# Performance work log

Hardware: AMD Instinct MI355X
Metric: run time of the kernel (lower is better)

The kernel has to match this reference:

```python
import jax, jax.numpy as jnp
from jax import lax
import numpy as np
import math

B, L = 256, 20000
HEADS, HEAD_DIM = 5, 30
W_POOL = (L - 10) // 5 + 1  # 3999, feature dim entering attention
ALPHA = 0.2  # tf.nn.leaky_relu default


def setup_inputs() -> dict:
    key = jax.random.key(0)
    ks = jax.random.split(key, 16)
    n = lambda k, shape: jax.random.normal(k, shape, dtype=jnp.float32) * 0.05
    return {
        "tokens": jax.random.randint(ks[0], (B, L), 0, 4, dtype=jnp.int32),
        "conv1_w": n(ks[1], (4, 10, 1, 5)),   # HWIO
        "conv1_b": jnp.zeros((5,), jnp.float32),
        "conv2_w": n(ks[2], (4, 10, 5, 1)),
        "conv2_b": jnp.zeros((1,), jnp.float32),
        "Wq": n(ks[3], (HEADS, W_POOL, HEAD_DIM)),
        "Wk": n(ks[4], (HEADS, W_POOL, HEAD_DIM)),
        "Wv": n(ks[5], (HEADS, W_POOL, HEAD_DIM)),
        "Wo": n(ks[6], (HEADS * HEAD_DIM, HEAD_DIM)),
        "d1_w": n(ks[7], (4 * HEAD_DIM, 10)),
        "d1_b": jnp.zeros((10,), jnp.float32),
        "d2_w": n(ks[8], (10, 10)),
        "d2_b": jnp.zeros((10,), jnp.float32),
        "d3_w": n(ks[9], (10, 1)),
        "d3_b": jnp.zeros((1,), jnp.float32),
    }


def _forward(tokens, conv1_w, conv1_b, conv2_w, conv2_b,
             Wq, Wk, Wv, Wo, d1_w, d1_b, d2_w, d2_b, d3_w, d3_b):
    dn = ("NHWC", "HWIO", "NHWC")
    # one_hot along axis 1: [B,4,L] -> NHWC image [B,4,L,1]
    x = jax.nn.one_hot(tokens, 4, axis=1, dtype=jnp.float32)[..., None]
    x = lax.conv_general_dilated(x, conv1_w, (1, 1), "SAME", dimension_numbers=dn) + conv1_b
    x = lax.conv_general_dilated(x, conv2_w, (1, 1), "SAME", dimension_numbers=dn) + conv2_b
    # MaxPool2D pool=(1,10), stride=(1,5), VALID -> [B,4,W_POOL,1]
    x = lax.reduce_window(x, -jnp.inf, lax.max, (1, 1, 10, 1), (1, 1, 5, 1), "VALID")
    x = x.reshape(x.shape[0], 4, -1)  # [B, S=4, D=W_POOL]
    S = x.shape[1]
    # batched multi-head causal self-attention (fused over heads)
    q = jnp.einsum("bsd,hde->bhse", x, Wq)
    k = jnp.einsum("bsd,hde->bhse", x, Wk)
    v = jnp.einsum("bsd,hde->bhse", x, Wv)
    scores = jnp.einsum("bhse,bhte->bhst", q, k) / math.sqrt(HEAD_DIM)
    mask = jnp.triu(jnp.full((S, S), -jnp.inf, dtype=jnp.float32), k=1)
    attn = jax.nn.softmax(scores + mask, axis=-1)
    o = jnp.einsum("bhst,bhte->bshe", attn, v).reshape(x.shape[0], S, HEADS * HEAD_DIM)
    o = o @ Wo  # [B, 4, 30]
    h = o.reshape(o.shape[0], -1)  # flatten -> [B, 120]
    h = jax.nn.leaky_relu(h @ d1_w + d1_b, ALPHA)
    h = jax.nn.leaky_relu(h @ d2_w + d2_b, ALPHA)
    return jax.nn.sigmoid(h @ d3_w + d3_b)  # [B, 1]


def reference(tokens, conv1_w, conv1_b, conv2_w, conv2_b,
              Wq, Wk, Wv, Wo, d1_w, d1_b, d2_w, d2_b, d3_w, d3_b):
    return _forward(tokens, conv1_w, conv1_b, conv2_w, conv2_b,
                    Wq, Wk, Wv, Wo, d1_w, d1_b, d2_w, d2_b, d3_w, d3_b)
```

## Files before the change

### kernel.cpp

```cpp
#include <hip/hip_runtime.h>
#include <math.h>

#define Bb 256
#define Ll 20000
#define WPOOL 3999
#define HEADS 5
#define HDIM 30
#define KSPLIT 8
#define NQKV 450
#define PSTRIDE (NQKV*1024)
#define BQT 4
#define WTRS 480
#define NB_K1 (Bb*16)

#define WS_F    0
#define WS_BIAS 368
#define WS_G    384
#define WS_FBL  1288
#define WS_FBR  2728
#define WS_BBL  4528
#define WS_BBR  4544
#define WS_X    4608
#define WS_P    (WS_X + Bb*WPOOL*4)
#define WS_WT   (WS_P + KSPLIT*PSTRIDE)

__device__ __forceinline__ float tbl_entry(const float* __restrict__ WP,
    int t, int d, int i, int kw2min, int kw2max)
{
    if (t >= 4) return 0.f;
    float p[4] = {0.f, 0.f, 0.f, 0.f};
#pragma unroll
    for (int kh = 0; kh < 4; ++kh) {
        int r = i + kh - 1;
        if (r < 0 || r > 3) continue;
        int kh1 = t - r + 1;
        if (kh1 < 0 || kh1 > 3) continue;
        int lo = d - kw2max; if (lo < 0) lo = 0;
        int hi = d - kw2min; if (hi > 9) hi = 9;
        const float* wpa = WP + (kh1 * 10) * 40 + kh * 10;
        for (int kw1 = lo; kw1 <= hi; ++kw1)
            p[kh] += wpa[kw1 * 40 + (d - kw1)];
    }
    return (p[0] + p[1]) + (p[2] + p[3]);
}

__global__ __launch_bounds__(256) void k0_build(const float* __restrict__ w1g,
    const float* __restrict__ b1g, const float* __restrict__ w2g,
    const float* __restrict__ b2g, float* __restrict__ ws)
{
    __shared__ float w1[200], w2[200], b1[5], WP[1600], SB[40], Fsh[360];
    __shared__ float b2v;
    const int tid = threadIdx.x;

    for (int i = tid; i < 200; i += 256) {
        w1[i] = w1g[i];
        w2[i] = w2g[i];
    }
    if (tid < 5) b1[tid] = b1g[tid];
    if (tid == 5) b2v = b2g[0];
    __syncthreads();

    for (int idx = tid; idx < 1600; idx += 256) {
        int a = idx / 40, b = idx % 40;
        float acc = 0.f;
#pragma unroll
        for (int c = 0; c < 5; ++c) acc += w1[a * 5 + c] * w2[b * 5 + c];
        WP[idx] = acc;
    }
    if (tid < 40) {
        float acc = 0.f;
#pragma unroll
        for (int c = 0; c < 5; ++c) acc += b1[c] * w2[tid * 5 + c];
        SB[tid] = acc;
    }
    __syncthreads();

    if (blockIdx.x == 0) {
        for (int idx = tid; idx < 360; idx += 256) {
            int t = idx / 72, d = (idx / 4) % 18, i = idx % 4;
            float v = tbl_entry(WP, t, d, i, 0, 9);
            Fsh[idx] = v;
            ws[WS_F + idx] = v;
        }
        if (tid < 4) {
            int i = tid;
            float acc = b2v;
#pragma unroll
            for (int kh = 0; kh < 4; ++kh) {
                int r = i + kh - 1;
                if (r < 0 || r > 3) continue;
                for (int kw2 = 0; kw2 < 10; ++kw2) acc += SB[kh * 10 + kw2];
            }
            ws[WS_BIAS + i] = acc;
        }
        __syncthreads();
        for (int idx = tid; idx < 900; idx += 256) {
            int p = idx / 36, j = (idx / 4) % 9, i = idx % 4;
            int t0 = p / 5, t1 = p % 5;
            ws[WS_G + idx] = Fsh[(t0 * 18 + 2 * j) * 4 + i]
                           + Fsh[(t1 * 18 + 2 * j + 1) * 4 + i];
        }
    } else {
        int gidx = (blockIdx.x - 1) * 256 + tid;
        if (gidx < 3240) {
            int wslot = gidx / 360, rem = gidx % 360;
            int t = rem / 72, d = (rem / 4) % 18, i = rem % 4;
            bool left = wslot < 4;
            int wloc = left ? wslot : wslot - 4;
            int kw2min = left ? 4 - wloc : 0;
            int kw2max = left ? 9 : 8 - wloc;
            float v = tbl_entry(WP, t, d, i, kw2min, kw2max);
            ws[(left ? WS_FBL + wloc * 360 : WS_FBR + wloc * 360) + rem] = v;
        } else if (gidx < 3276) {
            int bs = gidx - 3240;
            int wslot = bs / 4, i = bs % 4;
            bool left = wslot < 4;
            int wloc = left ? wslot : wslot - 4;
            int kw2min = left ? 4 - wloc : 0;
            int kw2max = left ? 9 : 8 - wloc;
            float acc = b2v;
#pragma unroll
            for (int kh = 0; kh < 4; ++kh) {
                int r = i + kh - 1;
                if (r < 0 || r > 3) continue;
                for (int kw2 = kw2min; kw2 <= kw2max; ++kw2)
                    acc += SB[kh * 10 + kw2];
            }
            ws[(left ? WS_BBL + wloc * 4 : WS_BBR + wloc * 4) + i] = acc;
        }
    }
}

__global__ __launch_bounds__(256) void k1_convpool(const int* __restrict__ tokens,
    const float* __restrict__ Wq, const float* __restrict__ Wk,
    const float* __restrict__ Wv, const float* __restrict__ ws_c,
    float* __restrict__ ws)
{
    __shared__ int tok[1280];
    __shared__ float4 Gs[225];
    __shared__ float4 m5[256];
    __shared__ float4 biasS;

    const int tid = threadIdx.x;

    if (blockIdx.x >= NB_K1) {
        int idx = (blockIdx.x - NB_K1) * 256 + tid;
        if (idx < WPOOL * WTRS) {
            int k = idx / WTRS, slot = idx % WTRS;
            int t = slot >> 2, c = slot & 3;
            int ph = t >> 3, j = t & 7;
            int proj = ph / 5, hh = ph % 5;
            float v = 0.f;
            int e = (j < 7) ? 4 * j + c : 28 + c;
            if (e < 30) {
                const float* Wm = (proj == 0) ? Wq : ((proj == 1) ? Wk : Wv);
                v = Wm[(size_t)hh * WPOOL * 30 + (size_t)k * 30 + e];
            }
            ws[WS_WT + idx] = v;
        }
        return;
    }

    const int b = blockIdx.x >> 4;
    const int chunk = blockIdx.x & 15;
    const int p0 = chunk * 250;
    const int pcnt = min(250, WPOOL - p0);
    const int colBase = 5 * p0 - 8;

    const float4* Gg = reinterpret_cast<const float4*>(ws_c + WS_G);
    for (int j = tid; j < 225; j += 256) Gs[j] = Gg[j];
    if (tid == 0) biasS = *reinterpret_cast<const float4*>(ws_c + WS_BIAS);
    const int* tb = tokens + (size_t)b * Ll;
    for (int j = tid; j < 1280; j += 256) {
        int u = colBase + j;
        tok[j] = (u >= 0 && u < Ll) ? tb[u] : 4;
    }
    __syncthreads();

    if (tid <= pcnt) {
        const int W = 5 * (p0 + tid);
        int tk[22];
#pragma unroll
        for (int m = 0; m < 22; ++m) tk[m] = tok[5 * tid + m];

        float4 mymax;
        const bool isLeft = (chunk == 0 && tid == 0);
        const bool isRight = (W + 4 >= Ll - 5);
        if (!isLeft && !isRight) {
            float4 bias4 = biasS;
            bool first = true;
#pragma unroll
            for (int c = 0; c < 5; ++c) {
                float a0 = bias4.x, a1 = bias4.y, a2 = bias4.z, a3 = bias4.w;
#pragma unroll
                for (int j = 0; j < 9; ++j) {
                    int pc = tk[c + 2 * j] * 5 + tk[c + 2 * j + 1];
                    float4 g = Gs[pc * 9 + j];
                    a0 += g.x; a1 += g.y; a2 += g.z; a3 += g.w;
                }
                if (first) { mymax = make_float4(a0, a1, a2, a3); first = false; }
                else {
                    mymax.x = fmaxf(mymax.x, a0); mymax.y = fmaxf(mymax.y, a1);
                    mymax.z = fmaxf(mymax.z, a2); mymax.w = fmaxf(mymax.w, a3);
                }
            }
        } else {
            bool first = true;
            for (int c = 0; c < 5; ++c) {
                int w = W + c;
                const float* T; const float* Bv;
                if (w < 4)            { T = ws_c + WS_FBL + w * 360;           Bv = ws_c + WS_BBL + 4 * w; }
                else if (w >= Ll - 5) { T = ws_c + WS_FBR + (w - (Ll - 5)) * 360; Bv = ws_c + WS_BBR + 4 * (w - (Ll - 5)); }
                else                  { T = ws_c + WS_F;                        Bv = ws_c + WS_BIAS; }
                float a0 = Bv[0], a1 = Bv[1], a2 = Bv[2], a3 = Bv[3];
                for (int d = 0; d < 18; ++d) {
                    const float* f = T + (size_t)(tk[c + d] * 18 + d) * 4;
                    a0 += f[0]; a1 += f[1]; a2 += f[2]; a3 += f[3];
                }
                if (first) { mymax = make_float4(a0, a1, a2, a3); first = false; }
                else {
                    mymax.x = fmaxf(mymax.x, a0); mymax.y = fmaxf(mymax.y, a1);
                    mymax.z = fmaxf(mymax.z, a2); mymax.w = fmaxf(mymax.w, a3);
                }
            }
        }
        m5[tid] = mymax;
    }
    __syncthreads();

    if (tid < pcnt) {
        float4 a = m5[tid], c = m5[tid + 1];
        a.x = fmaxf(a.x, c.x); a.y = fmaxf(a.y, c.y);
        a.z = fmaxf(a.z, c.z); a.w = fmaxf(a.w, c.w);
        reinterpret_cast<float4*>(ws + WS_X)[(size_t)b * WPOOL + p0 + tid] = a;
    }
}

__global__ __launch_bounds__(512) void k2_qkv(const float* __restrict__ xbuf,
    const float* __restrict__ wtbuf, float* __restrict__ ws)
{
    __shared__ float red[120 * 65];
    const int tid = threadIdx.x;
    const int ks = blockIdx.x & 7;
    const int bt = blockIdx.x >> 3;
    const int bq0 = bt * BQT;
    const int k0 = ks * 500;
    const int kn = min(500, WPOOL - k0);

    const int grp = tid >> 7;
    const int t = tid & 127;
    const int gk0 = __builtin_amdgcn_readfirstlane(grp) * 125;
    const int gend = min(gk0 + 125, kn);

    const int ph = t >> 3, j = t & 7;
    const int proj = ph / 5, hh = ph % 5;
    const int e0 = (j < 7) ? 4 * j : 28;
    const bool quad = (j < 7);
    const float* wt = wtbuf + (size_t)k0 * WTRS + 4 * t;
    const float4* xg[BQT];
#pragma unroll
    for (int b = 0; b < BQT; ++b)
        xg[b] = reinterpret_cast<const float4*>(xbuf)
                + (size_t)(bq0 + b) * WPOOL + k0;

    float acc[BQT][4][4] = {};

#define FMA_STEP(KIDX, W) do {                                       \
        _Pragma("unroll")                                            \
        for (int b = 0; b < BQT; ++b) {                              \
            float4 xv = xg[b][KIDX];                                 \
            acc[b][0][0] = fmaf(xv.x, W.x, acc[b][0][0]);            \
            acc[b][1][0] = fmaf(xv.y, W.x, acc[b][1][0]);            \
            acc[b][2][0] = fmaf(xv.z, W.x, acc[b][2][0]);            \
            acc[b][3][0] = fmaf(xv.w, W.x, acc[b][3][0]);            \
            acc[b][0][1] = fmaf(xv.x, W.y, acc[b][0][1]);            \
            acc[b][1][1] = fmaf(xv.y, W.y, acc[b][1][1]);            \
            acc[b][2][1] = fmaf(xv.z, W.y, acc[b][2][1]);            \
            acc[b][3][1] = fmaf(xv.w, W.y, acc[b][3][1]);            \
            acc[b][0][2] = fmaf(xv.x, W.z, acc[b][0][2]);            \
            acc[b][1][2] = fmaf(xv.y, W.z, acc[b][1][2]);            \
            acc[b][2][2] = fmaf(xv.z, W.z, acc[b][2][2]);            \
            acc[b][3][2] = fmaf(xv.w, W.z, acc[b][3][2]);            \
            acc[b][0][3] = fmaf(xv.x, W.w, acc[b][0][3]);            \
            acc[b][1][3] = fmaf(xv.y, W.w, acc[b][1][3]);            \
            acc[b][2][3] = fmaf(xv.z, W.w, acc[b][2][3]);            \
            acc[b][3][3] = fmaf(xv.w, W.w, acc[b][3][3]);            \
        }                                                            \
    } while (0)

    if (t < 120) {
        float4 wv[4];
#pragma unroll
        for (int i = 0; i < 4; ++i)
            wv[i] = *reinterpret_cast<const float4*>(wt + (size_t)(gk0 + i) * WTRS);

        int kk = gk0;
        for (; kk + 4 <= gend; kk += 4) {
#pragma unroll
            for (int i = 0; i < 4; ++i) {
                float4 W = wv[i];
                int nidx = kk + 4 + i;
                int ncl = nidx < gend ? nidx : gend - 1;
                wv[i] = *reinterpret_cast<const float4*>(wt + (size_t)ncl * WTRS);
                FMA_STEP(kk + i, W);
            }
        }
        for (; kk < gend; ++kk) {
            float4 W = *reinterpret_cast<const float4*>(wt + (size_t)kk * WTRS);
            FMA_STEP(kk, W);
        }
    }
#undef FMA_STEP

    __syncthreads();
#pragma unroll
    for (int g = 1; g < 4; ++g) {
        if (grp == g && t < 120) {
#pragma unroll
            for (int b = 0; b < BQT; ++b)
#pragma unroll
                for (int s = 0; s < 4; ++s)
#pragma unroll
                    for (int jj = 0; jj < 4; ++jj)
                        red[t * 65 + b * 16 + s * 4 + jj] = acc[b][s][jj];
        }
        __syncthreads();
        if (grp == 0 && t < 120) {
#pragma unroll
            for (int b = 0; b < BQT; ++b)
#pragma unroll
                for (int s = 0; s < 4; ++s)
#pragma unroll
                    for (int jj = 0; jj < 4; ++jj)
                        acc[b][s][jj] += red[t * 65 + b * 16 + s * 4 + jj];
        }
        __syncthreads();
    }

    if (grp == 0 && t < 120) {
        const int n0 = proj * 150 + hh * 30 + e0;
        float* Pb = ws + WS_P + (size_t)ks * PSTRIDE;
#pragma unroll
        for (int b = 0; b < BQT; ++b) {
#pragma unroll
            for (int s = 0; s < 4; ++s) {
                float* p = Pb + (size_t)(bq0 + b) * 1800 + s * 450 + n0;
                reinterpret_cast<float2*>(p)[0] = make_float2(acc[b][s][0], acc[b][s][1]);
                if (quad)
                    reinterpret_cast<float2*>(p + 2)[0] = make_float2(acc[b][s][2], acc[b][s][3]);
            }
        }
    }
}

__global__ __launch_bounds__(256) void k3_attn(const float* __restrict__ Wo,
    const float* __restrict__ d1w, const float* __restrict__ d1b,
    const float* __restrict__ d2w, const float* __restrict__ d2b,
    const float* __restrict__ d3w, const float* __restrict__ d3b,
    const float* __restrict__ ws, float* __restrict__ out)
{
    __shared__ float Qs[5][4][30], Ks2[5][4][30], Vs[5][4][30];
    __shared__ float sc[5][4][4];
    __shared__ float ob[4][150];
    __shared__ float hb[120], h1[10], h2[10];
    const int tid = threadIdx.x;
    const int b = blockIdx.x;
    const float* P = ws + WS_P + (size_t)b * 1800;

    for (int idx = tid; idx < 1800; idx += 256) {
        float val = 0.f;
#pragma unroll
        for (int ks = 0; ks < KSPLIT; ++ks)
            val += P[(size_t)ks * PSTRIDE + idx];
        int s = idx / 450, n = idx % 450;
        int proj = n / 150, hh = (n % 150) / 30, e = n % 30;
        if (proj == 0)      Qs[hh][s][e] = val;
        else if (proj == 1) Ks2[hh][s][e] = val;
        else                Vs[hh][s][e] = val;
    }
    __syncthreads();

    if (tid < 80) {
        int hh = tid >> 4, s = (tid >> 2) & 3, t = tid & 3;
        float a = 0.f;
        if (t <= s) {
            for (int e = 0; e < 30; ++e) a += Qs[hh][s][e] * Ks2[hh][t][e];
            a *= (1.0f / sqrtf(30.0f));
        }
        sc[hh][s][t] = a;
    }
    __syncthreads();

    if (tid < 20) {
        int hh = tid / 4, s = tid % 4;
        float m = -1e30f;
        for (int t = 0; t <= s; ++t) m = fmaxf(m, sc[hh][s][t]);
        float ex[4]; float den = 0.f;
        for (int t = 0; t <= s; ++t) { ex[t] = expf(sc[hh][s][t] - m); den += ex[t]; }
        for (int t = 0; t < 4; ++t) sc[hh][s][t] = (t <= s) ? ex[t] / den : 0.f;
    }
    __syncthreads();

    for (int idx = tid; idx < 600; idx += 256) {
        int s = idx / 150, j = idx % 150, hh = j / 30, e = j % 30;
        float a = 0.f;
        for (int t = 0; t < 4; ++t) a += sc[hh][s][t] * Vs[hh][t][e];
        ob[s][j] = a;
    }
    __syncthreads();

    if (tid < 120) {
        int s = tid / 30, e2 = tid % 30;
        float a = 0.f;
        for (int j = 0; j < 150; ++j) a += ob[s][j] * Wo[j * 30 + e2];
        hb[s * 30 + e2] = a;
    }
    __syncthreads();

    if (tid < 10) {
        float a = d1b[tid];
        for (int i = 0; i < 120; ++i) a += hb[i] * d1w[i * 10 + tid];
        h1[tid] = a > 0.f ? a : 0.2f * a;
    }
    __syncthreads();
    if (tid < 10) {
        float a = d2b[tid];
        for (int i = 0; i < 10; ++i) a += h1[i] * d2w[i * 10 + tid];
        h2[tid] = a > 0.f ? a : 0.2f * a;
    }
    __syncthreads();
    if (tid == 0) {
        float a = d3b[0];
        for (int i = 0; i < 10; ++i) a += h2[i] * d3w[i];
        out[b] = 1.f / (1.f + expf(-a));
    }
}

extern "C" void kernel_launch(void* const* d_in, const int* in_sizes, int n_in,
                              void* d_out, int out_size, void* d_ws, size_t ws_size,
                              hipStream_t stream)
{
    const int*   tokens = (const int*)d_in[0];
    const float* c1w = (const float*)d_in[1];
    const float* c1b = (const float*)d_in[2];
    const float* c2w = (const float*)d_in[3];
    const float* c2b = (const float*)d_in[4];
    const float* Wq  = (const float*)d_in[5];
    const float* Wk  = (const float*)d_in[6];
    const float* Wv  = (const float*)d_in[7];
    const float* Wo  = (const float*)d_in[8];
    const float* d1w = (const float*)d_in[9];
    const float* d1b = (const float*)d_in[10];
    const float* d2w = (const float*)d_in[11];
    const float* d2b = (const float*)d_in[12];
    const float* d3w = (const float*)d_in[13];
    const float* d3b = (const float*)d_in[14];
    float* ws = (float*)d_ws;
    float* out = (float*)d_out;

    const int transwBlocks = (WPOOL * WTRS + 255) / 256;
    k0_build<<<14, 256, 0, stream>>>(c1w, c1b, c2w, c2b, ws);
    k1_convpool<<<NB_K1 + transwBlocks, 256, 0, stream>>>(tokens, Wq, Wk, Wv, ws, ws);
    k2_qkv<<<(Bb / BQT) * KSPLIT, 512, 0, stream>>>(ws + WS_X, ws + WS_WT, ws);
    k3_attn<<<Bb, 256, 0, stream>>>(Wo, d1w, d1b, d2w, d2b, d3w, d3b, ws, out);
}
```

Baseline: 102.2 us.

## Replace FP32 QKV projection with bf16 MFMA GEMM over padded operands

The FP32 FMA kernel for the QKV projection is replaced by a bf16 MFMA GEMM (16x16x32) with a 4-way K split. The conv/pool kernel now also writes a bf16 copy of the pooled activations, padded to K=4096. Extra blocks convert Wq/Wk/Wv into a transposed, zero-padded bf16 layout. This aims to cut the projection's compute and memory time using matrix cores, at the cost of bf16 rounding error and per-call weight conversion.

```diff
diff --git a/kernel.cpp b/kernel.cpp
--- a/kernel.cpp
+++ b/kernel.cpp
@@ -6,12 +6,11 @@
 #define WPOOL 3999
 #define HEADS 5
 #define HDIM 30
-#define KSPLIT 8
-#define NQKV 450
-#define PSTRIDE (NQKV*1024)
-#define BQT 4
-#define WTRS 480
 #define NB_K1 (Bb*16)
+#define WBBLK 960
+#define PADABLK 388
+#define MKS 4
+#define PS2 (Bb*1800)
 
 #define WS_F    0
 #define WS_BIAS 368
@@ -22,7 +21,16 @@
 #define WS_BBR  4544
 #define WS_X    4608
 #define WS_P    (WS_X + Bb*WPOOL*4)
-#define WS_WT   (WS_P + KSPLIT*PSTRIDE)
+#define WS_A    (WS_P + MKS*PS2)
+#define WS_WB   (WS_A + 1024*4096/2)
+
+typedef short short8 __attribute__((ext_vector_type(8)));
+typedef float f32x4 __attribute__((ext_vector_type(4)));
+
+__device__ __forceinline__ unsigned short f2bf(float f) {
+    unsigned u = __float_as_uint(f);
+    return (unsigned short)((u + 0x7FFFu + ((u >> 16) & 1u)) >> 16);
+}
 
 __device__ __forceinline__ float tbl_entry(const float* __restrict__ WP,
     int t, int d, int i, int kw2min, int kw2max)
@@ -144,19 +152,40 @@
     const int tid = threadIdx.x;
 
     if (blockIdx.x >= NB_K1) {
-        int idx = (blockIdx.x - NB_K1) * 256 + tid;
-        if (idx < WPOOL * WTRS) {
-            int k = idx / WTRS, slot = idx % WTRS;
-            int t = slot >> 2, c = slot & 3;
-            int ph = t >> 3, j = t & 7;
-            int proj = ph / 5, hh = ph % 5;
-            float v = 0.f;
-            int e = (j < 7) ? 4 * j + c : 28 + c;
-            if (e < 30) {
+        int xb = blockIdx.x - NB_K1;
+        unsigned short* Au = reinterpret_cast<unsigned short*>(ws + WS_A);
+        unsigned short* WBu = reinterpret_cast<unsigned short*>(ws + WS_WB);
+        if (xb < WBBLK) {
+            int idx = xb * 256 + tid;
+            int n = idx >> 9;
+            int k0 = (idx & 511) * 8;
+            unsigned short vals[8];
+            if (n < 450) {
+                int proj = n / 150, hh = (n % 150) / 30, e = n % 30;
                 const float* Wm = (proj == 0) ? Wq : ((proj == 1) ? Wk : Wv);
-                v = Wm[(size_t)hh * WPOOL * 30 + (size_t)k * 30 + e];
-            }
-            ws[WS_WT + idx] = v;
+                const float* base = Wm + (size_t)hh * WPOOL * 30 + e;
+#pragma unroll
+                for (int j = 0; j < 8; ++j) {
+                    int k = k0 + j;
+                    vals[j] = (k < WPOOL) ? f2bf(base[(size_t)k * 30]) : (unsigned short)0;
+                }
+            } else {
+#pragma unroll
+                for (int j = 0; j < 8; ++j) vals[j] = 0;
+            }
+            unsigned w0 = (unsigned)vals[0] | ((unsigned)vals[1] << 16);
+            unsigned w1 = (unsigned)vals[2] | ((unsigned)vals[3] << 16);
+            unsigned w2 = (unsigned)vals[4] | ((unsigned)vals[5] << 16);
+            unsigned w3 = (unsigned)vals[6] | ((unsigned)vals[7] << 16);
+            *reinterpret_cast<uint4*>(WBu + (size_t)n * 4096 + k0) =
+                make_uint4(w0, w1, w2, w3);
+        } else {
+            int idx = (xb - WBBLK) * 256 + tid;
+            if (idx < 1024 * 97) {
+                int row = idx / 97;
+                int kk = WPOOL + idx % 97;
+                Au[(size_t)row * 4096 + kk] = 0;
+            }
         }
         return;
     }
@@ -232,125 +261,69 @@
         float4 a = m5[tid], c = m5[tid + 1];
         a.x = fmaxf(a.x, c.x); a.y = fmaxf(a.y, c.y);
         a.z = fmaxf(a.z, c.z); a.w = fmaxf(a.w, c.w);
-        reinterpret_cast<float4*>(ws + WS_X)[(size_t)b * WPOOL + p0 + tid] = a;
-    }
-}
-
-__global__ __launch_bounds__(512) void k2_qkv(const float* __restrict__ xbuf,
-    const float* __restrict__ wtbuf, float* __restrict__ ws)
-{
-    __shared__ float red[120 * 65];
-    const int tid = threadIdx.x;
-    const int ks = blockIdx.x & 7;
-    const int bt = blockIdx.x >> 3;
-    const int bq0 = bt * BQT;
-    const int k0 = ks * 500;
-    const int kn = min(500, WPOOL - k0);
-
-    const int grp = tid >> 7;
-    const int t = tid & 127;
-    const int gk0 = __builtin_amdgcn_readfirstlane(grp) * 125;
-    const int gend = min(gk0 + 125, kn);
-
-    const int ph = t >> 3, j = t & 7;
-    const int proj = ph / 5, hh = ph % 5;
-    const int e0 = (j < 7) ? 4 * j : 28;
-    const bool quad = (j < 7);
-    const float* wt = wtbuf + (size_t)k0 * WTRS + 4 * t;
-    const float4* xg[BQT];
-#pragma unroll
-    for (int b = 0; b < BQT; ++b)
-        xg[b] = reinterpret_cast<const float4*>(xbuf)
-                + (size_t)(bq0 + b) * WPOOL + k0;
-
-    float acc[BQT][4][4] = {};
-
-#define FMA_STEP(KIDX, W) do {                                       \
-        _Pragma("unroll")                                            \
-        for (int b = 0; b < BQT; ++b) {                              \
-            float4 xv = xg[b][KIDX];                                 \
-            acc[b][0][0] = fmaf(xv.x, W.x, acc[b][0][0]);            \
-            acc[b][1][0] = fmaf(xv.y, W.x, acc[b][1][0]);            \
-            acc[b][2][0] = fmaf(xv.z, W.x, acc[b][2][0]);            \
-            acc[b][3][0] = fmaf(xv.w, W.x, acc[b][3][0]);            \
-            acc[b][0][1] = fmaf(xv.x, W.y, acc[b][0][1]);            \
-            acc[b][1][1] = fmaf(xv.y, W.y, acc[b][1][1]);            \
-            acc[b][2][1] = fmaf(xv.z, W.y, acc[b][2][1]);            \
-            acc[b][3][1] = fmaf(xv.w, W.y, acc[b][3][1]);            \
-            acc[b][0][2] = fmaf(xv.x, W.z, acc[b][0][2]);            \
-            acc[b][1][2] = fmaf(xv.y, W.z, acc[b][1][2]);            \
-            acc[b][2][2] = fmaf(xv.z, W.z, acc[b][2][2]);            \
-            acc[b][3][2] = fmaf(xv.w, W.z, acc[b][3][2]);            \
-            acc[b][0][3] = fmaf(xv.x, W.w, acc[b][0][3]);            \
-            acc[b][1][3] = fmaf(xv.y, W.w, acc[b][1][3]);            \
-            acc[b][2][3] = fmaf(xv.z, W.w, acc[b][2][3]);            \
-            acc[b][3][3] = fmaf(xv.w, W.w, acc[b][3][3]);            \
-        }                                                            \
+        const int k = p0 + tid;
+        reinterpret_cast<float4*>(ws + WS_X)[(size_t)b * WPOOL + k] = a;
+        unsigned short* Au = reinterpret_cast<unsigned short*>(ws + WS_A);
+        Au[(size_t)(b * 4 + 0) * 4096 + k] = f2bf(a.x);
+        Au[(size_t)(b * 4 + 1) * 4096 + k] = f2bf(a.y);
+        Au[(size_t)(b * 4 + 2) * 4096 + k] = f2bf(a.z);
+        Au[(size_t)(b * 4 + 3) * 4096 + k] = f2bf(a.w);
+    }
+}
+
+__global__ __launch_bounds__(256) void k2_mfma(const unsigned short* __restrict__ A,
+    const unsigned short* __restrict__ WB, float* __restrict__ P)
+{
+    const int wave = threadIdx.x >> 6;
+    const int lane = threadIdx.x & 63;
+    const int mg = blockIdx.x & 15;
+    const int rest = blockIdx.x >> 4;
+    const int ng = rest % 6;
+    const int ks = rest / 6;
+    const int m0 = (mg * 4 + wave) * 16;
+    const int n0 = ng * 80;
+    const int kbase = ks * 1024;
+
+    const int lrow = lane & 15;
+    const int lk = (lane >> 4) * 8;
+
+    const unsigned short* Ap = A + (size_t)(m0 + lrow) * 4096 + kbase + lk;
+    const unsigned short* Bp = WB + (size_t)(n0 + lrow) * 4096 + kbase + lk;
+
+    f32x4 acc0 = {0.f, 0.f, 0.f, 0.f};
+    f32x4 acc1 = acc0, acc2 = acc0, acc3 = acc0, acc4 = acc0;
+
+#pragma unroll 4
+    for (int step = 0; step < 32; ++step) {
+        const unsigned short* ap = Ap + step * 32;
+        const unsigned short* bp = Bp + step * 32;
+        short8 af = *reinterpret_cast<const short8*>(ap);
+        short8 b0 = *reinterpret_cast<const short8*>(bp);
+        short8 b1 = *reinterpret_cast<const short8*>(bp + (size_t)16 * 4096);
+        short8 b2 = *reinterpret_cast<const short8*>(bp + (size_t)32 * 4096);
+        short8 b3 = *reinterpret_cast<const short8*>(bp + (size_t)48 * 4096);
+        short8 b4 = *reinterpret_cast<const short8*>(bp + (size_t)64 * 4096);
+        acc0 = __builtin_amdgcn_mfma_f32_16x16x32_bf16(af, b0, acc0, 0, 0, 0);
+        acc1 = __builtin_amdgcn_mfma_f32_16x16x32_bf16(af, b1, acc1, 0, 0, 0);
+        acc2 = __builtin_amdgcn_mfma_f32_16x16x32_bf16(af, b2, acc2, 0, 0, 0);
+        acc3 = __builtin_amdgcn_mfma_f32_16x16x32_bf16(af, b3, acc3, 0, 0, 0);
+        acc4 = __builtin_amdgcn_mfma_f32_16x16x32_bf16(af, b4, acc4, 0, 0, 0);
+    }
+
+    const int rbase = (lane >> 4) * 4;
+    float* Pb = P + (size_t)ks * PS2;
+#define STORE(ACC, T) do {                                              \
+        int col = n0 + (T) * 16 + lrow;                                 \
+        if (col < 450) {                                                \
+            _Pragma("unroll")                                           \
+            for (int r = 0; r < 4; ++r) {                               \
+                int m = m0 + rbase + r;                                 \
+                Pb[(size_t)(m >> 2) * 1800 + (m & 3) * 450 + col] = ACC[r]; \
+            }                                                           \
+        }                                                               \
     } while (0)
-
-    if (t < 120) {
-        float4 wv[4];
-#pragma unroll
-        for (int i = 0; i < 4; ++i)
-            wv[i] = *reinterpret_cast<const float4*>(wt + (size_t)(gk0 + i) * WTRS);
-
-        int kk = gk0;
-        for (; kk + 4 <= gend; kk += 4) {
-#pragma unroll
-            for (int i = 0; i < 4; ++i) {
-                float4 W = wv[i];
-                int nidx = kk + 4 + i;
-                int ncl = nidx < gend ? nidx : gend - 1;
-                wv[i] = *reinterpret_cast<const float4*>(wt + (size_t)ncl * WTRS);
-                FMA_STEP(kk + i, W);
-            }
-        }
-        for (; kk < gend; ++kk) {
-            float4 W = *reinterpret_cast<const float4*>(wt + (size_t)kk * WTRS);
-            FMA_STEP(kk, W);
-        }
-    }
-#undef FMA_STEP
-
-    __syncthreads();
-#pragma unroll
-    for (int g = 1; g < 4; ++g) {
-        if (grp == g && t < 120) {
-#pragma unroll
-            for (int b = 0; b < BQT; ++b)
-#pragma unroll
-                for (int s = 0; s < 4; ++s)
-#pragma unroll
-                    for (int jj = 0; jj < 4; ++jj)
-                        red[t * 65 + b * 16 + s * 4 + jj] = acc[b][s][jj];
-        }
-        __syncthreads();
-        if (grp == 0 && t < 120) {
-#pragma unroll
-            for (int b = 0; b < BQT; ++b)
-#pragma unroll
-                for (int s = 0; s < 4; ++s)
-#pragma unroll
-                    for (int jj = 0; jj < 4; ++jj)
-                        acc[b][s][jj] += red[t * 65 + b * 16 + s * 4 + jj];
-        }
-        __syncthreads();
-    }
-
-    if (grp == 0 && t < 120) {
-        const int n0 = proj * 150 + hh * 30 + e0;
-        float* Pb = ws + WS_P + (size_t)ks * PSTRIDE;
-#pragma unroll
-        for (int b = 0; b < BQT; ++b) {
-#pragma unroll
-            for (int s = 0; s < 4; ++s) {
-                float* p = Pb + (size_t)(bq0 + b) * 1800 + s * 450 + n0;
-                reinterpret_cast<float2*>(p)[0] = make_float2(acc[b][s][0], acc[b][s][1]);
-                if (quad)
-                    reinterpret_cast<float2*>(p + 2)[0] = make_float2(acc[b][s][2], acc[b][s][3]);
-            }
-        }
-    }
+    STORE(acc0, 0); STORE(acc1, 1); STORE(acc2, 2); STORE(acc3, 3); STORE(acc4, 4);
+#undef STORE
 }
 
 __global__ __launch_bounds__(256) void k3_attn(const float* __restrict__ Wo,
@@ -370,8 +343,8 @@
     for (int idx = tid; idx < 1800; idx += 256) {
         float val = 0.f;
 #pragma unroll
-        for (int ks = 0; ks < KSPLIT; ++ks)
-            val += P[(size_t)ks * PSTRIDE + idx];
+        for (int ks = 0; ks < MKS; ++ks)
+            val += P[(size_t)ks * PS2 + idx];
         int s = idx / 450, n = idx % 450;
         int proj = n / 150, hh = (n % 150) / 30, e = n % 30;
         if (proj == 0)      Qs[hh][s][e] = val;
@@ -458,9 +431,11 @@
     float* ws = (float*)d_ws;
     float* out = (float*)d_out;
 
-    const int transwBlocks = (WPOOL * WTRS + 255) / 256;
     k0_build<<<14, 256, 0, stream>>>(c1w, c1b, c2w, c2b, ws);
-    k1_convpool<<<NB_K1 + transwBlocks, 256, 0, stream>>>(tokens, Wq, Wk, Wv, ws, ws);
-    k2_qkv<<<(Bb / BQT) * KSPLIT, 512, 0, stream>>>(ws + WS_X, ws + WS_WT, ws);
+    k1_convpool<<<NB_K1 + WBBLK + PADABLK, 256, 0, stream>>>(tokens, Wq, Wk, Wv, ws, ws);
+    k2_mfma<<<16 * 6 * MKS, 256, 0, stream>>>(
+        reinterpret_cast<const unsigned short*>(ws + WS_A),
+        reinterpret_cast<const unsigned short*>(ws + WS_WB),
+        ws + WS_P);
     k3_attn<<<Bb, 256, 0, stream>>>(Wo, d1w, d1b, d2w, d2b, d3w, d3b, ws, out);
 }
```

Measured after the change: 101.1 us. Within noise of the previous version (-1.1%).
